# Kernel tuning notes

Hardware: AMD Instinct MI355X
Metric: run time of the kernel (lower is better)

## Reference

```python
import jax, jax.numpy as jnp
import numpy as np

B, T, V, E, H, S = 256, 512, 10000, 512, 1024, 64


def _lin(k, out_dim, in_dim):
    kw, kb = jax.random.split(k)
    bound = 1.0 / np.sqrt(in_dim)
    W = jax.random.uniform(kw, (out_dim, in_dim), jnp.float32, -bound, bound)
    b = jax.random.uniform(kb, (out_dim,), jnp.float32, -bound, bound)
    return W, b


def setup_inputs() -> dict:
    key = jax.random.key(0)
    ks = jax.random.split(key, 16)
    labels = jax.random.randint(ks[0], (B, T), 0, V)
    deltas = jax.random.uniform(ks[1], (B, T), jnp.float32)
    lengths = jax.random.randint(ks[2], (B,), 0, T)
    state_features = jax.random.normal(ks[3], (B, S), jnp.float32)
    emb = jax.random.normal(ks[4], (V, E), jnp.float32) * 0.02
    emb = emb.at[0].set(0.0)  # padding_idx=0
    proj_W, proj_b = _lin(ks[5], H, E + 2)
    dec_W, dec_b = _lin(ks[6], H, 1)
    bound = 1.0 / np.sqrt(H)
    W_ih = jax.random.uniform(ks[7], (4 * H, H), jnp.float32, -bound, bound)
    W_hh = jax.random.uniform(ks[8], (4 * H, H), jnp.float32, -bound, bound)
    b_ih = jax.random.uniform(ks[9], (4 * H,), jnp.float32, -bound, bound)
    b_hh = jax.random.uniform(ks[10], (4 * H,), jnp.float32, -bound, bound)
    sh1_W, sh1_b = _lin(ks[11], H, H + S)
    sh2_W, sh2_b = _lin(ks[12], H, H)
    lab_W, lab_b = _lin(ks[13], V, H)
    del_W, del_b = _lin(ks[14], 1, H)
    return dict(labels=labels, deltas=deltas, lengths=lengths,
                state_features=state_features, emb=emb,
                proj_W=proj_W, proj_b=proj_b, dec_W=dec_W, dec_b=dec_b,
                W_ih=W_ih, W_hh=W_hh, b_ih=b_ih, b_hh=b_hh,
                sh1_W=sh1_W, sh1_b=sh1_b, sh2_W=sh2_W, sh2_b=sh2_b,
                lab_W=lab_W, lab_b=lab_b, del_W=del_W, del_b=del_b)


def reference(labels, deltas, lengths, state_features, emb,
              proj_W, proj_b, dec_W, dec_b,
              W_ih, W_hh, b_ih, b_hh,
              sh1_W, sh1_b, sh2_W, sh2_b,
              lab_W, lab_b, del_W, del_b):
    valid = jnp.arange(T)[None, :] < lengths[:, None]  # [B,T] bool

    def step(carry, x):
        h, c = carry
        lab_t, d_t, v_t = x                      # [B], [B], [B]
        dlog = jnp.log1p(d_t)[:, None]           # [B,1]
        e = emb[lab_t]                           # [B,E]
        gamma = jax.nn.sigmoid(dlog @ dec_W.T + dec_b)
        h = h * gamma
        inp = jnp.concatenate([e, dlog, v_t[:, None].astype(e.dtype)], axis=-1)
        xp = inp @ proj_W.T + proj_b             # [B,H]
        gates = xp @ W_ih.T + b_ih + h @ W_hh.T + b_hh  # [B,4H] (i,f,g,o)
        i, f, g, o = jnp.split(gates, 4, axis=-1)
        nc = jax.nn.sigmoid(f) * c + jax.nn.sigmoid(i) * jnp.tanh(g)
        nh = jax.nn.sigmoid(o) * jnp.tanh(nc)
        m = v_t[:, None]
        h = jnp.where(m, nh, h)
        c = jnp.where(m, nc, c)
        return (h, c), None

    h0 = jnp.zeros((B, H), jnp.float32)
    c0 = jnp.zeros((B, H), jnp.float32)
    xs = (labels.T, deltas.T, valid.T)           # leading time axis
    (h, c), _ = jax.lax.scan(step, (h0, c0), xs)
    t = jnp.concatenate([h, state_features], axis=-1)
    t = jax.nn.relu(t @ sh1_W.T + sh1_b)
    t = jax.nn.relu(t @ sh2_W.T + sh2_b)
    return t @ lab_W.T + lab_b, (t @ del_W.T + del_b)[:, 0]
```

## Files before the change

### kernel.cpp

```cpp
#include <hip/hip_runtime.h>

typedef __bf16 bf16;
typedef __bf16 bf16x8 __attribute__((ext_vector_type(8)));
typedef float f32x4 __attribute__((ext_vector_type(4)));

#define AS1 __attribute__((address_space(1)))
#define AS3 __attribute__((address_space(3)))

__device__ __forceinline__ void glds16(const void* src, void* lds) {
  __builtin_amdgcn_global_load_lds((const AS1 unsigned*)src, (AS3 unsigned*)lds, 16, 0, 0);
}
__device__ __forceinline__ float sigm(float x) { return 1.f / (1.f + __expf(-x)); }
__device__ __forceinline__ float tanh_f(float x) {
  float ax = fabsf(x);
  float e = __expf(-2.f * ax);
  float t = (1.f - e) / (1.f + e);
  return x < 0.f ? -t : t;
}
__device__ __forceinline__ float bits2f(unsigned u) {
  union { unsigned u; float f; } c; c.u = u; return c.f;
}
__device__ __forceinline__ void mfma_va(f32x4& acc, bf16x8 a, const f32x4& b_agpr) {
  asm("v_mfma_f32_16x16x32_bf16 %0, %1, %2, %0" : "+v"(acc) : "v"(a), "a"(b_agpr));
}

template<bool OUT_BF, bool RELU, bool HAS_BIAS>
__global__ __launch_bounds__(256) void gemm_bt(
    const bf16* __restrict__ A, int lda,
    const bf16* __restrict__ B, int ldb,
    void* __restrict__ Cv, int ldc,
    const float* __restrict__ bias,
    int M, int N, int K)
{
  __shared__ __align__(16) char smA[8192];
  __shared__ __align__(16) char smB[8192];
  const int tid = threadIdx.x;
  const int l = tid & 63, w = tid >> 6;
  const int lo16 = l & 15, grp = l >> 4;
  const int m0 = blockIdx.x * 128, n0 = blockIdx.y * 128;
  const int wm = w & 1, wn = w >> 1;
  f32x4 acc[4][4] = {};
  for (int k0 = 0; k0 < K; k0 += 32) {
#pragma unroll
    for (int q = 0; q < 2; ++q) {
      const int c = w * 2 + q;
      const int alin = c * 1024 + l * 16;
      const int row = alin >> 6;
      const int sb = alin ^ (((row >> 1) & 3) << 4);
      const int kk = (sb & 63) >> 1;
      int ra = m0 + row; ra = ra < M ? ra : M - 1;
      glds16(A + (size_t)ra * lda + k0 + kk, smA + c * 1024);
      int rb = n0 + row; rb = rb < N ? rb : N - 1;
      glds16(B + (size_t)rb * ldb + k0 + kk, smB + c * 1024);
    }
    __syncthreads();
    bf16x8 af[4], bfr[4];
#pragma unroll
    for (int mi = 0; mi < 4; ++mi) {
      int row = wm * 64 + mi * 16 + lo16;
      int a = ((row << 6) | (grp << 4)) ^ (((row >> 1) & 3) << 4);
      af[mi] = *(const bf16x8*)(smA + a);
    }
#pragma unroll
    for (int ni = 0; ni < 4; ++ni) {
      int row = wn * 64 + ni * 16 + lo16;
      int a = ((row << 6) | (grp << 4)) ^ (((row >> 1) & 3) << 4);
      bfr[ni] = *(const bf16x8*)(smB + a);
    }
#pragma unroll
    for (int mi = 0; mi < 4; ++mi)
#pragma unroll
      for (int ni = 0; ni < 4; ++ni)
        acc[mi][ni] = __builtin_amdgcn_mfma_f32_16x16x32_bf16(af[mi], bfr[ni], acc[mi][ni], 0, 0, 0);
    __syncthreads();
  }
#pragma unroll
  for (int mi = 0; mi < 4; ++mi)
#pragma unroll
    for (int ni = 0; ni < 4; ++ni)
#pragma unroll
      for (int r = 0; r < 4; ++r) {
        int row = m0 + wm * 64 + mi * 16 + grp * 4 + r;
        int col = n0 + wn * 64 + ni * 16 + lo16;
        if (row < M && col < N) {
          float v = acc[mi][ni][r];
          if (HAS_BIAS) v += bias[col];
          if (RELU) v = v > 0.f ? v : 0.f;
          if (OUT_BF) ((bf16*)Cv)[(size_t)row * ldc + col] = (bf16)v;
          else        ((float*)Cv)[(size_t)row * ldc + col] = v;
        }
      }
}

__global__ void conv_bf(const float* __restrict__ s, bf16* __restrict__ d, int n) {
  int i = blockIdx.x * 256 + threadIdx.x;
  if (i < n) d[i] = (bf16)s[i];
}

__global__ void dlog_prep(const float* __restrict__ deltas, float* __restrict__ dlog, int n) {
  int i = blockIdx.x * 256 + threadIdx.x;
  if (i < n) dlog[i] = log1pf(deltas[i]);
}

__global__ void build_projT(const float* __restrict__ projW, const float* __restrict__ projb,
                            bf16* __restrict__ pT) {
  int i = blockIdx.x * 256 + threadIdx.x;
  if (i >= 515 * 1024) return;
  int e = i >> 10, h = i & 1023;
  float v = (e < 514) ? projW[h * 514 + e] : projb[h];
  pT[i] = (bf16)v;
}

__global__ void wf_split(const float* __restrict__ wfused, const float* __restrict__ bih,
                         const float* __restrict__ bhh, float* __restrict__ wD,
                         float* __restrict__ wV, float* __restrict__ bias4) {
  int n = blockIdx.x * 256 + threadIdx.x;
  if (n >= 4096) return;
  wD[n] = wfused[(size_t)n * 520 + 512];
  wV[n] = wfused[(size_t)n * 520 + 513];
  bias4[n] = wfused[(size_t)n * 520 + 514] + bih[n] + bhh[n];
}
__global__ void wfe_conv(const float* __restrict__ wfused, bf16* __restrict__ wfe) {
  int i = blockIdx.x * 256 + threadIdx.x;
  if (i >= 4096 * 512) return;
  int n = i >> 9, e = i & 511;
  wfe[i] = (bf16)wfused[(size_t)n * 520 + e];
}

__global__ void prep_warr(const float* __restrict__ whh, bf16* __restrict__ warr) {
  int idx = blockIdx.x * 256 + threadIdx.x;
  if (idx >= 524288) return;
  int lx = idx & 63;
  int rest = idx >> 6;
  int nf = rest & 1; rest >>= 1;
  int q = rest & 15; rest >>= 4;
  int kh = rest & 1; rest >>= 1;
  int gg = rest & 3; rest >>= 2;
  int ng = rest;
  int row = gg * 1024 + ng * 32 + nf * 16 + (lx & 15);
  int kb = (q * 2 + kh) * 32 + (lx >> 4) * 8;
  bf16* dst = warr + (size_t)idx * 8;
  const float* src = whh + (size_t)row * 1024 + kb;
#pragma unroll
  for (int j = 0; j < 8; ++j) dst[j] = (bf16)src[j];
}

__global__ void build_tin(const float* __restrict__ hstate, const float* __restrict__ statef,
                          bf16* __restrict__ tin) {
  int i = blockIdx.x * 256 + threadIdx.x;
  if (i >= 256 * 1088) return;
  int b = i / 1088, k = i % 1088;
  float v = (k < 1024) ? hstate[b * 1024 + k] : statef[b * 64 + (k - 1024)];
  tin[i] = (bf16)v;
}

__global__ void delta_head(const bf16* __restrict__ t2, const float* __restrict__ delW,
                           const float* __restrict__ delb, float* __restrict__ out) {
  int b = threadIdx.x;
  float s = 0.f;
  for (int k = 0; k < 1024; ++k) s += (float)t2[b * 1024 + k] * delW[k];
  out[b] = s + delb[0];
}

__global__ void sentinel(float* out) { out[0] = 1e30f; }

__global__ __launch_bounds__(512, 2) void scan_kernel(
    const bf16* __restrict__ embg,
    const bf16* __restrict__ warr,
    const float* __restrict__ wfD, const float* __restrict__ wfV, const float* __restrict__ bias4,
    const int* __restrict__ labels, const float* __restrict__ dlog, const int* __restrict__ lengths,
    const float* __restrict__ decW, const float* __restrict__ decb,
    bf16* __restrict__ hpre0, bf16* __restrict__ hpre1,
    float* __restrict__ hstate, int* __restrict__ flags)
{
  __shared__ __align__(16) char smh[65536];
  __shared__ float smG[2][4][32][34];
  __shared__ float s_dl0[32], s_dl1[32];
  __shared__ int s_labN[32];

  const int tid = threadIdx.x;
  const int l = tid & 63, w = tid >> 6;
  const int lo16 = l & 15, grp = l >> 4;
  const int wg = blockIdx.x;
  const int ng = wg & 31, bg = wg >> 5;
  const int b0 = bg * 32, n0 = ng * 32;
  const int g = w & 3, kh = w >> 2;

  f32x4 wf[32];
  {
    const bf16* wp = warr + ((size_t)((ng * 4 + g) * 2 + kh)) * 16384 + (size_t)l * 8;
#pragma unroll
    for (int qq = 0; qq < 32; ++qq) wf[qq] = *(const f32x4*)(wp + (size_t)qq * 512);
#pragma unroll
    for (int qq = 0; qq < 32; ++qq)
      asm volatile("" : "+a"(wf[qq]));
  }

  const int row = tid >> 4;
  const int cp = tid & 15;
  const int c0 = cp * 2;
  const int len = lengths[b0 + row];
  const float dW0 = decW[n0 + c0], dW1 = decW[n0 + c0 + 1];
  const float dB0 = decb[n0 + c0], dB1 = decb[n0 + c0 + 1];
  float wD[4][2], wV[4][2], wB[4][2];
#pragma unroll
  for (int gg = 0; gg < 4; ++gg) {
    int cx = gg * 1024 + n0 + c0;
    wD[gg][0] = wfD[cx]; wD[gg][1] = wfD[cx + 1];
    wV[gg][0] = wfV[cx]; wV[gg][1] = wfV[cx + 1];
    wB[gg][0] = bias4[cx]; wB[gg][1] = bias4[cx + 1];
  }
  float cc0 = 0.f, cc1 = 0.f, hh0 = 0.f, hh1 = 0.f;
  int* grpflags = flags + bg * 32;

  float eg[4][2];
  {
    const int lab0 = labels[(b0 + row) * 512];
    const char* gb = (const char*)(embg + (size_t)lab0 * 4096 + n0 + c0);
#pragma unroll
    for (int gg = 0; gg < 4; ++gg) {
      unsigned u = *(const unsigned*)(gb + gg * 2048);
      eg[gg][0] = bits2f(u << 16);
      eg[gg][1] = bits2f(u & 0xffff0000u);
    }
  }

#pragma unroll 1
  for (int t = 0; t < 512; ++t) {
    const bf16* hread = (t & 1) ? hpre1 : hpre0;
    bf16* hwrite = (t & 1) ? hpre0 : hpre1;

    if (tid < 32) s_dl0[tid] = dlog[(b0 + tid) * 512 + t];
    else if (tid < 64) { int i = tid - 32; s_dl1[i] = (t + 1 < 512) ? dlog[(b0 + i) * 512 + t + 1] : 0.f; }
    else if (tid < 96) { int i = tid - 64; s_labN[i] = (t + 1 < 512) ? labels[(b0 + i) * 512 + t + 1] : 0; }

    if (t > 0) {
      f32x4 stg[8];
#pragma unroll
      for (int q = 0; q < 8; ++q) {
        const int r_ = 4 * w + (q >> 1);
        const int cb = (q & 1) * 1024 + l * 16;
        const char* src = (const char*)hread + (size_t)(b0 + r_) * 2048 + cb;
        asm volatile("global_load_dwordx4 %0, %1, off sc0 sc1" : "=v"(stg[q]) : "v"(src));
      }
      asm volatile("s_waitcnt vmcnt(0)" ::: "memory");
      __builtin_amdgcn_sched_barrier(0);
#pragma unroll
      for (int q = 0; q < 8; ++q) {
        const int r_ = 4 * w + (q >> 1);
        const int a = r_ * 2048 + (q & 1) * 1024 + l * 16;
        *(f32x4*)(smh + (a ^ ((r_ & 7) << 4))) = stg[q];
      }
    }
    __syncthreads();

    f32x4 a00 = {}, a01 = {}, a10 = {}, a11 = {};
    if (t > 0) {
#pragma unroll
      for (int q = 0; q < 16; ++q) {
        const int kf = q * 2 + kh;
        {
          const int ar = lo16;
          const int a = ((ar << 11) | (kf << 6) | (grp << 4)) ^ ((ar & 7) << 4);
          bf16x8 af = *(const bf16x8*)(smh + a);
          mfma_va(a00, af, wf[q * 2 + 0]);
          mfma_va(a01, af, wf[q * 2 + 1]);
        }
        {
          const int ar = 16 + lo16;
          const int a = ((ar << 11) | (kf << 6) | (grp << 4)) ^ ((ar & 7) << 4);
          bf16x8 af = *(const bf16x8*)(smh + a);
          mfma_va(a10, af, wf[q * 2 + 0]);
          mfma_va(a11, af, wf[q * 2 + 1]);
        }
      }
    }
#pragma unroll
    for (int r = 0; r < 4; ++r) {
      smG[kh][g][grp * 4 + r][lo16] = a00[r];
      smG[kh][g][grp * 4 + r][16 + lo16] = a01[r];
      smG[kh][g][16 + grp * 4 + r][lo16] = a10[r];
      smG[kh][g][16 + grp * 4 + r][16 + lo16] = a11[r];
    }
    __syncthreads();

    const float dl0 = s_dl0[row];
    const bool valid = t < len;
    float z[4][2];
#pragma unroll
    for (int gg = 0; gg < 4; ++gg) {
#pragma unroll
      for (int jj = 0; jj < 2; ++jj)
        z[gg][jj] = smG[0][gg][row][c0 + jj] + smG[1][gg][row][c0 + jj] + eg[gg][jj]
                  + dl0 * wD[gg][jj] + (valid ? wV[gg][jj] : 0.f) + wB[gg][jj];
    }
    float gam0 = sigm(dl0 * dW0 + dB0), gam1 = sigm(dl0 * dW1 + dB1);
    float nc0 = sigm(z[1][0]) * cc0 + sigm(z[0][0]) * tanh_f(z[2][0]);
    float nc1 = sigm(z[1][1]) * cc1 + sigm(z[0][1]) * tanh_f(z[2][1]);
    float nh0 = sigm(z[3][0]) * tanh_f(nc0);
    float nh1 = sigm(z[3][1]) * tanh_f(nc1);
    float hn0 = valid ? nh0 : hh0 * gam0;
    float hn1 = valid ? nh1 : hh1 * gam1;
    cc0 = valid ? nc0 : cc0;  cc1 = valid ? nc1 : cc1;
    hh0 = hn0;  hh1 = hn1;

    if (t < 511) {
      const float dl1 = s_dl1[row];
      float p0 = hn0 * sigm(dl1 * dW0 + dB0);
      float p1 = hn1 * sigm(dl1 * dW1 + dB1);
      unsigned short x0 = __builtin_bit_cast(unsigned short, (bf16)p0);
      unsigned short x1 = __builtin_bit_cast(unsigned short, (bf16)p1);
      unsigned uval = (unsigned)x0 | ((unsigned)x1 << 16);
      char* dst = (char*)hwrite + (size_t)(b0 + row) * 2048 + (size_t)(n0 + c0) * 2;
      asm volatile("global_store_dword %0, %1, off sc0 sc1" :: "v"(dst), "v"(uval) : "memory");
      asm volatile("s_waitcnt vmcnt(0)" ::: "memory");
      __syncthreads();
      if (tid == 0) {
        int* fdst = grpflags + ng;
        int fval = t + 1;
        asm volatile("global_store_dword %0, %1, off sc0 sc1" :: "v"(fdst), "v"(fval) : "memory");
      }
      unsigned u0, u1, u2, u3;
      {
        const int lnext = s_labN[row];
        const bf16* gb = embg + (size_t)lnext * 4096 + n0 + c0;
        asm volatile("global_load_dword %0, %1, off" : "=v"(u0) : "v"(gb));
        asm volatile("global_load_dword %0, %1, off" : "=v"(u1) : "v"(gb + 1024));
        asm volatile("global_load_dword %0, %1, off" : "=v"(u2) : "v"(gb + 2048));
        asm volatile("global_load_dword %0, %1, off" : "=v"(u3) : "v"(gb + 3072));
      }
      if (tid < 64) {
        const int* fp = grpflags + (tid & 31);
        const int tgt = t + 1;
        while (true) {
          int v = __hip_atomic_load(fp, __ATOMIC_RELAXED, __HIP_MEMORY_SCOPE_AGENT);
          if (__all(v >= tgt)) break;
          __builtin_amdgcn_s_sleep(1);
        }
      }
      asm volatile("s_waitcnt vmcnt(0)" ::: "memory");
      eg[0][0] = bits2f(u0 << 16); eg[0][1] = bits2f(u0 & 0xffff0000u);
      eg[1][0] = bits2f(u1 << 16); eg[1][1] = bits2f(u1 & 0xffff0000u);
      eg[2][0] = bits2f(u2 << 16); eg[2][1] = bits2f(u2 & 0xffff0000u);
      eg[3][0] = bits2f(u3 << 16); eg[3][1] = bits2f(u3 & 0xffff0000u);
      __syncthreads();
    } else {
      float* dst = hstate + (size_t)(b0 + row) * 1024 + n0 + c0;
      dst[0] = hn0; dst[1] = hn1;
    }
  }
}

extern "C" void kernel_launch(void* const* d_in, const int* in_sizes, int n_in,
                              void* d_out, int out_size, void* d_ws, size_t ws_size,
                              hipStream_t stream) {
  const int*   labels = (const int*)d_in[0];
  const float* deltas = (const float*)d_in[1];
  const int*   lengths= (const int*)d_in[2];
  const float* statef = (const float*)d_in[3];
  const float* emb    = (const float*)d_in[4];
  const float* projW  = (const float*)d_in[5];
  const float* projb  = (const float*)d_in[6];
  const float* decW   = (const float*)d_in[7];
  const float* decb   = (const float*)d_in[8];
  const float* wih    = (const float*)d_in[9];
  const float* whh    = (const float*)d_in[10];
  const float* bih    = (const float*)d_in[11];
  const float* bhh    = (const float*)d_in[12];
  const float* sh1W   = (const float*)d_in[13];
  const float* sh1b   = (const float*)d_in[14];
  const float* sh2W   = (const float*)d_in[15];
  const float* sh2b   = (const float*)d_in[16];
  const float* labW   = (const float*)d_in[17];
  const float* labb   = (const float*)d_in[18];
  const float* delW   = (const float*)d_in[19];
  const float* delb   = (const float*)d_in[20];

  char* ws = (char*)d_ws;
  size_t off = 0;
  auto alloc = [&](size_t bytes) -> void* {
    void* p = ws + off;
    off += (bytes + 1023) & ~(size_t)1023;
    return p;
  };
  bf16*  emb_bf  = (bf16*)alloc((size_t)10000 * 512 * 2);
  bf16*  projT   = (bf16*)alloc((size_t)515 * 1024 * 2);
  bf16*  wih_bf  = (bf16*)alloc((size_t)4096 * 1024 * 2);
  float* wfused  = (float*)alloc((size_t)4096 * 520 * 4);
  bf16*  wfe     = (bf16*)alloc((size_t)4096 * 512 * 2);
  float* wfD     = (float*)alloc(4096 * 4);
  float* wfV     = (float*)alloc(4096 * 4);
  float* bias4   = (float*)alloc(4096 * 4);
  bf16*  embg    = (bf16*)alloc((size_t)10000 * 4096 * 2);
  bf16*  warr    = (bf16*)alloc((size_t)4096 * 1024 * 2);
  bf16*  hpre0   = (bf16*)alloc((size_t)256 * 1024 * 2);
  bf16*  hpre1   = (bf16*)alloc((size_t)256 * 1024 * 2);
  float* hstate  = (float*)alloc((size_t)256 * 1024 * 4);
  float* dlogb   = (float*)alloc((size_t)256 * 512 * 4);
  bf16*  tin     = (bf16*)alloc((size_t)256 * 1088 * 2);
  bf16*  t1      = (bf16*)alloc((size_t)256 * 1024 * 2);
  bf16*  t2      = (bf16*)alloc((size_t)256 * 1024 * 2);
  bf16*  sh1w_bf = (bf16*)alloc((size_t)1024 * 1088 * 2);
  bf16*  sh2w_bf = (bf16*)alloc((size_t)1024 * 1024 * 2);
  bf16*  labw_bf = (bf16*)alloc((size_t)10000 * 1024 * 2);
  int*   flags   = (int*)alloc(2048);

  if (off > ws_size) {
    sentinel<<<1, 1, 0, stream>>>((float*)d_out);
    return;
  }

  conv_bf<<<(5120000 + 255) / 256, 256, 0, stream>>>(emb, emb_bf, 5120000);
  build_projT<<<(515 * 1024 + 255) / 256, 256, 0, stream>>>(projW, projb, projT);
  conv_bf<<<(4194304 + 255) / 256, 256, 0, stream>>>(wih, wih_bf, 4194304);
  dlog_prep<<<(131072 + 255) / 256, 256, 0, stream>>>(deltas, dlogb, 131072);
  gemm_bt<false, false, false><<<dim3(32, 5), 256, 0, stream>>>(
      wih_bf, 1024, projT, 1024, (void*)wfused, 520, nullptr, 4096, 515, 1024);
  wf_split<<<16, 256, 0, stream>>>(wfused, bih, bhh, wfD, wfV, bias4);
  wfe_conv<<<(4096 * 512 + 255) / 256, 256, 0, stream>>>(wfused, wfe);
  gemm_bt<true, false, false><<<dim3(79, 32), 256, 0, stream>>>(
      emb_bf, 512, wfe, 512, (void*)embg, 4096, nullptr, 10000, 4096, 512);
  prep_warr<<<(524288 + 255) / 256, 256, 0, stream>>>(whh, warr);
  conv_bf<<<(1114112 + 255) / 256, 256, 0, stream>>>(sh1W, sh1w_bf, 1114112);
  conv_bf<<<(1048576 + 255) / 256, 256, 0, stream>>>(sh2W, sh2w_bf, 1048576);
  conv_bf<<<(10240000 + 255) / 256, 256, 0, stream>>>(labW, labw_bf, 10240000);

  hipMemsetAsync(flags, 0, 2048, stream);
  scan_kernel<<<256, 512, 0, stream>>>(embg, warr, wfD, wfV, bias4,
                                       labels, dlogb, lengths, decW, decb,
                                       hpre0, hpre1, hstate, flags);

  build_tin<<<(256 * 1088 + 255) / 256, 256, 0, stream>>>(hstate, statef, tin);
  gemm_bt<true, true, true><<<dim3(2, 8), 256, 0, stream>>>(
      tin, 1088, sh1w_bf, 1088, (void*)t1, 1024, sh1b, 256, 1024, 1088);
  gemm_bt<true, true, true><<<dim3(2, 8), 256, 0, stream>>>(
      t1, 1024, sh2w_bf, 1024, (void*)t2, 1024, sh2b, 256, 1024, 1024);
  gemm_bt<false, false, true><<<dim3(2, 79), 256, 0, stream>>>(
      t2, 1024, labw_bf, 1024, d_out, 10000, labb, 256, 10000, 1024);
  delta_head<<<1, 256, 0, stream>>>(t2, delW, delb, (float*)d_out + 2560000);
}
```

Measured before the change: 3.499 ms.

## Interleave two batch groups per workgroup in the LSTM scan to hide sync latency

Halves the scan grid so each workgroup owns two 32-row batch groups and alternates between them each timestep. The aim is for one group's cross-workgroup flag wait and h exchange to overlap with compute on the other group. The embedding gather for the current label is now issued alongside the h loads instead of being prefetched one step ahead. In exchange, only 128 workgroups run, so each does twice the MFMA and elementwise work per step serially, and parallelism drops.

New measurement: 8.183 ms. +133.9%, slower.

```diff
diff --git a/kernel.cpp b/kernel.cpp
--- a/kernel.cpp
+++ b/kernel.cpp
@@ -176,14 +176,14 @@
   __shared__ __align__(16) char smh[65536];
   __shared__ float smG[2][4][32][34];
   __shared__ float s_dl0[32], s_dl1[32];
-  __shared__ int s_labN[32];
+  __shared__ int s_lab[32];
 
   const int tid = threadIdx.x;
   const int l = tid & 63, w = tid >> 6;
   const int lo16 = l & 15, grp = l >> 4;
   const int wg = blockIdx.x;
-  const int ng = wg & 31, bg = wg >> 5;
-  const int b0 = bg * 32, n0 = ng * 32;
+  const int ng = wg & 31, pair = wg >> 5;
+  const int n0 = ng * 32;
   const int g = w & 3, kh = w >> 2;
 
   f32x4 wf[32];
@@ -199,7 +199,8 @@
   const int row = tid >> 4;
   const int cp = tid & 15;
   const int c0 = cp * 2;
-  const int len = lengths[b0 + row];
+  const int b0g[2] = {pair * 32, (pair + 4) * 32};
+  const int leng[2] = {lengths[b0g[0] + row], lengths[b0g[1] + row]};
   const float dW0 = decW[n0 + c0], dW1 = decW[n0 + c0 + 1];
   const float dB0 = decb[n0 + c0], dB1 = decb[n0 + c0 + 1];
   float wD[4][2], wV[4][2], wB[4][2];
@@ -210,143 +211,141 @@
     wV[gg][0] = wfV[cx]; wV[gg][1] = wfV[cx + 1];
     wB[gg][0] = bias4[cx]; wB[gg][1] = bias4[cx + 1];
   }
-  float cc0 = 0.f, cc1 = 0.f, hh0 = 0.f, hh1 = 0.f;
-  int* grpflags = flags + bg * 32;
-
-  float eg[4][2];
-  {
-    const int lab0 = labels[(b0 + row) * 512];
-    const char* gb = (const char*)(embg + (size_t)lab0 * 4096 + n0 + c0);
-#pragma unroll
-    for (int gg = 0; gg < 4; ++gg) {
-      unsigned u = *(const unsigned*)(gb + gg * 2048);
-      eg[gg][0] = bits2f(u << 16);
-      eg[gg][1] = bits2f(u & 0xffff0000u);
-    }
-  }
+  float hh[2][2] = {{0.f, 0.f}, {0.f, 0.f}};
+  float cc[2][2] = {{0.f, 0.f}, {0.f, 0.f}};
 
 #pragma unroll 1
   for (int t = 0; t < 512; ++t) {
     const bf16* hread = (t & 1) ? hpre1 : hpre0;
     bf16* hwrite = (t & 1) ? hpre0 : hpre1;
-
-    if (tid < 32) s_dl0[tid] = dlog[(b0 + tid) * 512 + t];
-    else if (tid < 64) { int i = tid - 32; s_dl1[i] = (t + 1 < 512) ? dlog[(b0 + i) * 512 + t + 1] : 0.f; }
-    else if (tid < 96) { int i = tid - 64; s_labN[i] = (t + 1 < 512) ? labels[(b0 + i) * 512 + t + 1] : 0; }
-
-    if (t > 0) {
+#pragma unroll
+    for (int gi = 0; gi < 2; ++gi) {
+      const int b0 = b0g[gi];
+      int* gf = flags + (gi ? (pair + 4) : pair) * 32;
+
+      if (tid < 32) s_dl0[tid] = dlog[(b0 + tid) * 512 + t];
+      else if (tid < 64) { int i = tid - 32; s_dl1[i] = (t + 1 < 512) ? dlog[(b0 + i) * 512 + t + 1] : 0.f; }
+      else if (tid < 96) { int i = tid - 64; s_lab[i] = labels[(b0 + i) * 512 + t]; }
+      if (t > 0 && tid < 64) {
+        const int* fp = gf + (tid & 31);
+        while (true) {
+          int v = __hip_atomic_load(fp, __ATOMIC_RELAXED, __HIP_MEMORY_SCOPE_AGENT);
+          if (__all(v >= t)) break;
+          __builtin_amdgcn_s_sleep(1);
+        }
+      }
+      __syncthreads();
+
       f32x4 stg[8];
-#pragma unroll
-      for (int q = 0; q < 8; ++q) {
-        const int r_ = 4 * w + (q >> 1);
-        const int cb = (q & 1) * 1024 + l * 16;
-        const char* src = (const char*)hread + (size_t)(b0 + r_) * 2048 + cb;
-        asm volatile("global_load_dwordx4 %0, %1, off sc0 sc1" : "=v"(stg[q]) : "v"(src));
-      }
-      asm volatile("s_waitcnt vmcnt(0)" ::: "memory");
-      __builtin_amdgcn_sched_barrier(0);
-#pragma unroll
-      for (int q = 0; q < 8; ++q) {
-        const int r_ = 4 * w + (q >> 1);
-        const int a = r_ * 2048 + (q & 1) * 1024 + l * 16;
-        *(f32x4*)(smh + (a ^ ((r_ & 7) << 4))) = stg[q];
-      }
-    }
-    __syncthreads();
-
-    f32x4 a00 = {}, a01 = {}, a10 = {}, a11 = {};
-    if (t > 0) {
-#pragma unroll
-      for (int q = 0; q < 16; ++q) {
-        const int kf = q * 2 + kh;
-        {
-          const int ar = lo16;
-          const int a = ((ar << 11) | (kf << 6) | (grp << 4)) ^ ((ar & 7) << 4);
-          bf16x8 af = *(const bf16x8*)(smh + a);
-          mfma_va(a00, af, wf[q * 2 + 0]);
-          mfma_va(a01, af, wf[q * 2 + 1]);
-        }
-        {
-          const int ar = 16 + lo16;
-          const int a = ((ar << 11) | (kf << 6) | (grp << 4)) ^ ((ar & 7) << 4);
-          bf16x8 af = *(const bf16x8*)(smh + a);
-          mfma_va(a10, af, wf[q * 2 + 0]);
-          mfma_va(a11, af, wf[q * 2 + 1]);
-        }
-      }
-    }
-#pragma unroll
-    for (int r = 0; r < 4; ++r) {
-      smG[kh][g][grp * 4 + r][lo16] = a00[r];
-      smG[kh][g][grp * 4 + r][16 + lo16] = a01[r];
-      smG[kh][g][16 + grp * 4 + r][lo16] = a10[r];
-      smG[kh][g][16 + grp * 4 + r][16 + lo16] = a11[r];
-    }
-    __syncthreads();
-
-    const float dl0 = s_dl0[row];
-    const bool valid = t < len;
-    float z[4][2];
-#pragma unroll
-    for (int gg = 0; gg < 4; ++gg) {
-#pragma unroll
-      for (int jj = 0; jj < 2; ++jj)
-        z[gg][jj] = smG[0][gg][row][c0 + jj] + smG[1][gg][row][c0 + jj] + eg[gg][jj]
-                  + dl0 * wD[gg][jj] + (valid ? wV[gg][jj] : 0.f) + wB[gg][jj];
-    }
-    float gam0 = sigm(dl0 * dW0 + dB0), gam1 = sigm(dl0 * dW1 + dB1);
-    float nc0 = sigm(z[1][0]) * cc0 + sigm(z[0][0]) * tanh_f(z[2][0]);
-    float nc1 = sigm(z[1][1]) * cc1 + sigm(z[0][1]) * tanh_f(z[2][1]);
-    float nh0 = sigm(z[3][0]) * tanh_f(nc0);
-    float nh1 = sigm(z[3][1]) * tanh_f(nc1);
-    float hn0 = valid ? nh0 : hh0 * gam0;
-    float hn1 = valid ? nh1 : hh1 * gam1;
-    cc0 = valid ? nc0 : cc0;  cc1 = valid ? nc1 : cc1;
-    hh0 = hn0;  hh1 = hn1;
-
-    if (t < 511) {
-      const float dl1 = s_dl1[row];
-      float p0 = hn0 * sigm(dl1 * dW0 + dB0);
-      float p1 = hn1 * sigm(dl1 * dW1 + dB1);
-      unsigned short x0 = __builtin_bit_cast(unsigned short, (bf16)p0);
-      unsigned short x1 = __builtin_bit_cast(unsigned short, (bf16)p1);
-      unsigned uval = (unsigned)x0 | ((unsigned)x1 << 16);
-      char* dst = (char*)hwrite + (size_t)(b0 + row) * 2048 + (size_t)(n0 + c0) * 2;
-      asm volatile("global_store_dword %0, %1, off sc0 sc1" :: "v"(dst), "v"(uval) : "memory");
-      asm volatile("s_waitcnt vmcnt(0)" ::: "memory");
-      __syncthreads();
-      if (tid == 0) {
-        int* fdst = grpflags + ng;
-        int fval = t + 1;
-        asm volatile("global_store_dword %0, %1, off sc0 sc1" :: "v"(fdst), "v"(fval) : "memory");
+      if (t > 0) {
+#pragma unroll
+        for (int q = 0; q < 8; ++q) {
+          const int r_ = 4 * w + (q >> 1);
+          const int cb = (q & 1) * 1024 + l * 16;
+          const char* src = (const char*)hread + (size_t)(b0 + r_) * 2048 + cb;
+          asm volatile("global_load_dwordx4 %0, %1, off sc0 sc1" : "=v"(stg[q]) : "v"(src));
+        }
       }
       unsigned u0, u1, u2, u3;
       {
-        const int lnext = s_labN[row];
-        const bf16* gb = embg + (size_t)lnext * 4096 + n0 + c0;
+        const int lb = s_lab[row];
+        const bf16* gb = embg + (size_t)lb * 4096 + n0 + c0;
         asm volatile("global_load_dword %0, %1, off" : "=v"(u0) : "v"(gb));
         asm volatile("global_load_dword %0, %1, off" : "=v"(u1) : "v"(gb + 1024));
         asm volatile("global_load_dword %0, %1, off" : "=v"(u2) : "v"(gb + 2048));
         asm volatile("global_load_dword %0, %1, off" : "=v"(u3) : "v"(gb + 3072));
       }
-      if (tid < 64) {
-        const int* fp = grpflags + (tid & 31);
-        const int tgt = t + 1;
-        while (true) {
-          int v = __hip_atomic_load(fp, __ATOMIC_RELAXED, __HIP_MEMORY_SCOPE_AGENT);
-          if (__all(v >= tgt)) break;
-          __builtin_amdgcn_s_sleep(1);
-        }
-      }
+      if (t > 0) {
+        asm volatile("s_waitcnt vmcnt(4)" ::: "memory");
+        __builtin_amdgcn_sched_barrier(0);
+#pragma unroll
+        for (int q = 0; q < 8; ++q) {
+          const int r_ = 4 * w + (q >> 1);
+          const int a = r_ * 2048 + (q & 1) * 1024 + l * 16;
+          *(f32x4*)(smh + (a ^ ((r_ & 7) << 4))) = stg[q];
+        }
+      }
+      __syncthreads();
+
+      f32x4 a00 = {}, a01 = {}, a10 = {}, a11 = {};
+      if (t > 0) {
+#pragma unroll
+        for (int q = 0; q < 16; ++q) {
+          const int kf = q * 2 + kh;
+          {
+            const int ar = lo16;
+            const int a = ((ar << 11) | (kf << 6) | (grp << 4)) ^ ((ar & 7) << 4);
+            bf16x8 af = *(const bf16x8*)(smh + a);
+            mfma_va(a00, af, wf[q * 2 + 0]);
+            mfma_va(a01, af, wf[q * 2 + 1]);
+          }
+          {
+            const int ar = 16 + lo16;
+            const int a = ((ar << 11) | (kf << 6) | (grp << 4)) ^ ((ar & 7) << 4);
+            bf16x8 af = *(const bf16x8*)(smh + a);
+            mfma_va(a10, af, wf[q * 2 + 0]);
+            mfma_va(a11, af, wf[q * 2 + 1]);
+          }
+        }
+      }
+#pragma unroll
+      for (int r = 0; r < 4; ++r) {
+        smG[kh][g][grp * 4 + r][lo16] = a00[r];
+        smG[kh][g][grp * 4 + r][16 + lo16] = a01[r];
+        smG[kh][g][16 + grp * 4 + r][lo16] = a10[r];
+        smG[kh][g][16 + grp * 4 + r][16 + lo16] = a11[r];
+      }
+      __syncthreads();
+
       asm volatile("s_waitcnt vmcnt(0)" ::: "memory");
+      float eg[4][2];
       eg[0][0] = bits2f(u0 << 16); eg[0][1] = bits2f(u0 & 0xffff0000u);
       eg[1][0] = bits2f(u1 << 16); eg[1][1] = bits2f(u1 & 0xffff0000u);
       eg[2][0] = bits2f(u2 << 16); eg[2][1] = bits2f(u2 & 0xffff0000u);
       eg[3][0] = bits2f(u3 << 16); eg[3][1] = bits2f(u3 & 0xffff0000u);
-      __syncthreads();
-    } else {
-      float* dst = hstate + (size_t)(b0 + row) * 1024 + n0 + c0;
-      dst[0] = hn0; dst[1] = hn1;
+
+      const float dl0 = s_dl0[row];
+      const bool valid = t < leng[gi];
+      float z[4][2];
+#pragma unroll
+      for (int gg = 0; gg < 4; ++gg) {
+#pragma unroll
+        for (int jj = 0; jj < 2; ++jj)
+          z[gg][jj] = smG[0][gg][row][c0 + jj] + smG[1][gg][row][c0 + jj] + eg[gg][jj]
+                    + dl0 * wD[gg][jj] + (valid ? wV[gg][jj] : 0.f) + wB[gg][jj];
+      }
+      float gam0 = sigm(dl0 * dW0 + dB0), gam1 = sigm(dl0 * dW1 + dB1);
+      float nc0 = sigm(z[1][0]) * cc[gi][0] + sigm(z[0][0]) * tanh_f(z[2][0]);
+      float nc1 = sigm(z[1][1]) * cc[gi][1] + sigm(z[0][1]) * tanh_f(z[2][1]);
+      float nh0 = sigm(z[3][0]) * tanh_f(nc0);
+      float nh1 = sigm(z[3][1]) * tanh_f(nc1);
+      float hn0 = valid ? nh0 : hh[gi][0] * gam0;
+      float hn1 = valid ? nh1 : hh[gi][1] * gam1;
+      cc[gi][0] = valid ? nc0 : cc[gi][0];
+      cc[gi][1] = valid ? nc1 : cc[gi][1];
+      hh[gi][0] = hn0;  hh[gi][1] = hn1;
+
+      if (t < 511) {
+        const float dl1 = s_dl1[row];
+        float p0 = hn0 * sigm(dl1 * dW0 + dB0);
+        float p1 = hn1 * sigm(dl1 * dW1 + dB1);
+        unsigned short x0 = __builtin_bit_cast(unsigned short, (bf16)p0);
+        unsigned short x1 = __builtin_bit_cast(unsigned short, (bf16)p1);
+        unsigned uval = (unsigned)x0 | ((unsigned)x1 << 16);
+        char* dst = (char*)hwrite + (size_t)(b0 + row) * 2048 + (size_t)(n0 + c0) * 2;
+        asm volatile("global_store_dword %0, %1, off sc0 sc1" :: "v"(dst), "v"(uval) : "memory");
+        asm volatile("s_waitcnt vmcnt(0)" ::: "memory");
+        __syncthreads();
+        if (tid == 0) {
+          int* fdst = gf + ng;
+          int fval = t + 1;
+          asm volatile("global_store_dword %0, %1, off sc0 sc1" :: "v"(fdst), "v"(fval) : "memory");
+        }
+      } else {
+        float* dst = hstate + (size_t)(b0 + row) * 1024 + n0 + c0;
+        dst[0] = hn0; dst[1] = hn1;
+        __syncthreads();
+      }
     }
   }
 }
@@ -426,7 +425,7 @@
   conv_bf<<<(10240000 + 255) / 256, 256, 0, stream>>>(labW, labw_bf, 10240000);
 
   hipMemsetAsync(flags, 0, 2048, stream);
-  scan_kernel<<<256, 512, 0, stream>>>(embg, warr, wfD, wfV, bias4,
+  scan_kernel<<<128, 512, 0, stream>>>(embg, warr, wfD, wfV, bias4,
                                        labels, dlogb, lengths, decW, decb,
                                        hpre0, hpre1, hstate, flags);
 
```

## Replace shared group flags with per-consumer flag slots and split h-load pipeline

Applied to the files above, without the earlier changes.

Replaces the per-group flag array polled with agent-scope atomics by per-consumer flag copies: each producer writes its step counter into 32 consumer-private slots (a cached copy plus a system-coherent fallback copy), and consumers poll their own slots at the start of the next step rather than at the end of the current one. The hidden-state load is split into two halves so the second half's LDS write overlaps the first half of the MFMA loop, and the embedding gather for the current step is issued alongside the h loads. This aims to reduce polling contention and the latency of the inter-block barrier, at the cost of more flag stores, an extra __syncthreads, and reliance on the non-coherent flag read eventually observing the update.

New measurement: 5.767 ms. 64.8% more time.

```diff
diff --git a/kernel.cpp b/kernel.cpp
--- a/kernel.cpp
+++ b/kernel.cpp
@@ -176,7 +176,7 @@
   __shared__ __align__(16) char smh[65536];
   __shared__ float smG[2][4][32][34];
   __shared__ float s_dl0[32], s_dl1[32];
-  __shared__ int s_labN[32];
+  __shared__ int s_lab[32];
 
   const int tid = threadIdx.x;
   const int l = tid & 63, w = tid >> 6;
@@ -211,19 +211,8 @@
     wB[gg][0] = bias4[cx]; wB[gg][1] = bias4[cx + 1];
   }
   float cc0 = 0.f, cc1 = 0.f, hh0 = 0.f, hh1 = 0.f;
-  int* grpflags = flags + bg * 32;
-
-  float eg[4][2];
-  {
-    const int lab0 = labels[(b0 + row) * 512];
-    const char* gb = (const char*)(embg + (size_t)lab0 * 4096 + n0 + c0);
-#pragma unroll
-    for (int gg = 0; gg < 4; ++gg) {
-      unsigned u = *(const unsigned*)(gb + gg * 2048);
-      eg[gg][0] = bits2f(u << 16);
-      eg[gg][1] = bits2f(u & 0xffff0000u);
-    }
-  }
+
+  const int cons_base = (bg * 32 + ng) * 32;
 
 #pragma unroll 1
   for (int t = 0; t < 512; ++t) {
@@ -232,24 +221,59 @@
 
     if (tid < 32) s_dl0[tid] = dlog[(b0 + tid) * 512 + t];
     else if (tid < 64) { int i = tid - 32; s_dl1[i] = (t + 1 < 512) ? dlog[(b0 + i) * 512 + t + 1] : 0.f; }
-    else if (tid < 96) { int i = tid - 64; s_labN[i] = (t + 1 < 512) ? labels[(b0 + i) * 512 + t + 1] : 0; }
+    else if (tid < 96) { int i = tid - 64; s_lab[i] = labels[(b0 + i) * 512 + t]; }
 
     if (t > 0) {
-      f32x4 stg[8];
-#pragma unroll
-      for (int q = 0; q < 8; ++q) {
-        const int r_ = 4 * w + (q >> 1);
-        const int cb = (q & 1) * 1024 + l * 16;
-        const char* src = (const char*)hread + (size_t)(b0 + r_) * 2048 + cb;
-        asm volatile("global_load_dwordx4 %0, %1, off sc0 sc1" : "=v"(stg[q]) : "v"(src));
-      }
-      asm volatile("s_waitcnt vmcnt(0)" ::: "memory");
+      const int* pp = flags + cons_base + (tid & 31);
+      const int* pd = flags + 8192 + cons_base + (tid & 31);
+      int it = 0;
+      while (true) {
+        int v;
+        asm volatile("global_load_dword %0, %1, off sc0" : "=v"(v) : "v"(pp));
+        asm volatile("s_waitcnt vmcnt(0)" ::: "memory");
+        if (__all(v >= t)) break;
+        if ((++it & 7) == 0) {
+          asm volatile("global_load_dword %0, %1, off sc0 sc1" : "=v"(v) : "v"(pd));
+          asm volatile("s_waitcnt vmcnt(0)" ::: "memory");
+          if (__all(v >= t)) break;
+        }
+        __builtin_amdgcn_s_sleep(1);
+      }
+    }
+
+    f32x4 stq[8];
+    if (t > 0) {
+#pragma unroll
+      for (int qi = 0; qi < 4; ++qi) {
+        const char* src = (const char*)hread + (size_t)(b0 + 4 * w + qi) * 2048 + l * 16;
+        asm volatile("global_load_dwordx4 %0, %1, off sc0 sc1" : "=v"(stq[qi]) : "v"(src));
+      }
+#pragma unroll
+      for (int qi = 0; qi < 4; ++qi) {
+        const char* src = (const char*)hread + (size_t)(b0 + 4 * w + qi) * 2048 + 1024 + l * 16;
+        asm volatile("global_load_dwordx4 %0, %1, off sc0 sc1" : "=v"(stq[4 + qi]) : "v"(src));
+      }
+    }
+    __syncthreads();
+
+    unsigned u0, u1, u2, u3;
+    {
+      const int lb = s_lab[row];
+      const bf16* gb = embg + (size_t)lb * 4096 + n0 + c0;
+      asm volatile("global_load_dword %0, %1, off" : "=v"(u0) : "v"(gb));
+      asm volatile("global_load_dword %0, %1, off" : "=v"(u1) : "v"(gb + 1024));
+      asm volatile("global_load_dword %0, %1, off" : "=v"(u2) : "v"(gb + 2048));
+      asm volatile("global_load_dword %0, %1, off" : "=v"(u3) : "v"(gb + 3072));
+    }
+
+    if (t > 0) {
+      asm volatile("s_waitcnt vmcnt(8)" ::: "memory");
       __builtin_amdgcn_sched_barrier(0);
 #pragma unroll
-      for (int q = 0; q < 8; ++q) {
-        const int r_ = 4 * w + (q >> 1);
-        const int a = r_ * 2048 + (q & 1) * 1024 + l * 16;
-        *(f32x4*)(smh + (a ^ ((r_ & 7) << 4))) = stg[q];
+      for (int qi = 0; qi < 4; ++qi) {
+        const int r_ = 4 * w + qi;
+        const int a = r_ * 2048 + l * 16;
+        *(f32x4*)(smh + (a ^ ((r_ & 7) << 4))) = stq[qi];
       }
     }
     __syncthreads();
@@ -257,7 +281,7 @@
     f32x4 a00 = {}, a01 = {}, a10 = {}, a11 = {};
     if (t > 0) {
 #pragma unroll
-      for (int q = 0; q < 16; ++q) {
+      for (int q = 0; q < 8; ++q) {
         const int kf = q * 2 + kh;
         {
           const int ar = lo16;
@@ -274,6 +298,36 @@
           mfma_va(a11, af, wf[q * 2 + 1]);
         }
       }
+      asm volatile("s_waitcnt vmcnt(4)" ::: "memory");
+      __builtin_amdgcn_sched_barrier(0);
+#pragma unroll
+      for (int qi = 0; qi < 4; ++qi) {
+        const int r_ = 4 * w + qi;
+        const int a = r_ * 2048 + 1024 + l * 16;
+        *(f32x4*)(smh + (a ^ ((r_ & 7) << 4))) = stq[4 + qi];
+      }
+    }
+    __syncthreads();
+
+    if (t > 0) {
+#pragma unroll
+      for (int q = 8; q < 16; ++q) {
+        const int kf = q * 2 + kh;
+        {
+          const int ar = lo16;
+          const int a = ((ar << 11) | (kf << 6) | (grp << 4)) ^ ((ar & 7) << 4);
+          bf16x8 af = *(const bf16x8*)(smh + a);
+          mfma_va(a00, af, wf[q * 2 + 0]);
+          mfma_va(a01, af, wf[q * 2 + 1]);
+        }
+        {
+          const int ar = 16 + lo16;
+          const int a = ((ar << 11) | (kf << 6) | (grp << 4)) ^ ((ar & 7) << 4);
+          bf16x8 af = *(const bf16x8*)(smh + a);
+          mfma_va(a10, af, wf[q * 2 + 0]);
+          mfma_va(a11, af, wf[q * 2 + 1]);
+        }
+      }
     }
 #pragma unroll
     for (int r = 0; r < 4; ++r) {
@@ -283,6 +337,13 @@
       smG[kh][g][16 + grp * 4 + r][16 + lo16] = a11[r];
     }
     __syncthreads();
+
+    asm volatile("s_waitcnt vmcnt(0)" ::: "memory");
+    float eg[4][2];
+    eg[0][0] = bits2f(u0 << 16); eg[0][1] = bits2f(u0 & 0xffff0000u);
+    eg[1][0] = bits2f(u1 << 16); eg[1][1] = bits2f(u1 & 0xffff0000u);
+    eg[2][0] = bits2f(u2 << 16); eg[2][1] = bits2f(u2 & 0xffff0000u);
+    eg[3][0] = bits2f(u3 << 16); eg[3][1] = bits2f(u3 & 0xffff0000u);
 
     const float dl0 = s_dl0[row];
     const bool valid = t < len;
@@ -315,35 +376,14 @@
       asm volatile("global_store_dword %0, %1, off sc0 sc1" :: "v"(dst), "v"(uval) : "memory");
       asm volatile("s_waitcnt vmcnt(0)" ::: "memory");
       __syncthreads();
-      if (tid == 0) {
-        int* fdst = grpflags + ng;
+      if (tid < 32) {
+        const int idx = (bg * 32 + tid) * 32 + ng;
+        int* fp = flags + idx;
+        int* fd = flags + 8192 + idx;
         int fval = t + 1;
-        asm volatile("global_store_dword %0, %1, off sc0 sc1" :: "v"(fdst), "v"(fval) : "memory");
-      }
-      unsigned u0, u1, u2, u3;
-      {
-        const int lnext = s_labN[row];
-        const bf16* gb = embg + (size_t)lnext * 4096 + n0 + c0;
-        asm volatile("global_load_dword %0, %1, off" : "=v"(u0) : "v"(gb));
-        asm volatile("global_load_dword %0, %1, off" : "=v"(u1) : "v"(gb + 1024));
-        asm volatile("global_load_dword %0, %1, off" : "=v"(u2) : "v"(gb + 2048));
-        asm volatile("global_load_dword %0, %1, off" : "=v"(u3) : "v"(gb + 3072));
-      }
-      if (tid < 64) {
-        const int* fp = grpflags + (tid & 31);
-        const int tgt = t + 1;
-        while (true) {
-          int v = __hip_atomic_load(fp, __ATOMIC_RELAXED, __HIP_MEMORY_SCOPE_AGENT);
-          if (__all(v >= tgt)) break;
-          __builtin_amdgcn_s_sleep(1);
-        }
-      }
-      asm volatile("s_waitcnt vmcnt(0)" ::: "memory");
-      eg[0][0] = bits2f(u0 << 16); eg[0][1] = bits2f(u0 & 0xffff0000u);
-      eg[1][0] = bits2f(u1 << 16); eg[1][1] = bits2f(u1 & 0xffff0000u);
-      eg[2][0] = bits2f(u2 << 16); eg[2][1] = bits2f(u2 & 0xffff0000u);
-      eg[3][0] = bits2f(u3 << 16); eg[3][1] = bits2f(u3 & 0xffff0000u);
-      __syncthreads();
+        asm volatile("global_store_dword %0, %1, off" :: "v"(fp), "v"(fval) : "memory");
+        asm volatile("global_store_dword %0, %1, off sc0 sc1" :: "v"(fd), "v"(fval) : "memory");
+      }
     } else {
       float* dst = hstate + (size_t)(b0 + row) * 1024 + n0 + c0;
       dst[0] = hn0; dst[1] = hn1;
@@ -403,7 +443,7 @@
   bf16*  sh1w_bf = (bf16*)alloc((size_t)1024 * 1088 * 2);
   bf16*  sh2w_bf = (bf16*)alloc((size_t)1024 * 1024 * 2);
   bf16*  labw_bf = (bf16*)alloc((size_t)10000 * 1024 * 2);
-  int*   flags   = (int*)alloc(2048);
+  int*   flags   = (int*)alloc(65536);
 
   if (off > ws_size) {
     sentinel<<<1, 1, 0, stream>>>((float*)d_out);
@@ -425,7 +465,7 @@
   conv_bf<<<(1048576 + 255) / 256, 256, 0, stream>>>(sh2W, sh2w_bf, 1048576);
   conv_bf<<<(10240000 + 255) / 256, 256, 0, stream>>>(labW, labw_bf, 10240000);
 
-  hipMemsetAsync(flags, 0, 2048, stream);
+  hipMemsetAsync(flags, 0, 65536, stream);
   scan_kernel<<<256, 512, 0, stream>>>(embg, warr, wfD, wfV, bias4,
                                        labels, dlogb, lengths, decW, decb,
                                        hpre0, hpre1, hstate, flags);
```
